# Kernel optimization log

Hardware: AMD Instinct MI355X
Metric: run time of the kernel (lower is better)

Reference implementation:

```python
import jax, jax.numpy as jnp
import numpy as np

NUM_GRAPHS = 256  # static batch size (= batch_indices.max()+1 by construction)
EMBED = 32
HIDDEN = 256
DEPTH = 10


def setup_inputs() -> dict:
    key = jax.random.key(0)
    ks = jax.random.split(key, 16)
    N, M = 8192, 16384
    atom_features = jax.random.randint(ks[0], (N,), 0, 200, dtype=jnp.int32)
    bond_features = jax.random.randint(ks[1], (M,), 0, 10, dtype=jnp.int32)
    adjacency_matrix = jax.random.randint(ks[2], (N, N), 0, 2, dtype=jnp.int32)
    batch_indices = jnp.sort(jax.random.randint(ks[3], (N,), 0, NUM_GRAPHS, dtype=jnp.int32))
    s = 0.05
    atom_emb_table = jax.random.normal(ks[4], (200, EMBED), jnp.float32) * s
    bond_emb_table = jax.random.normal(ks[5], (10, EMBED), jnp.float32) * s
    msg_W = jax.random.normal(ks[6], (DEPTH, HIDDEN, 2 * EMBED), jnp.float32) * s
    msg_b = jax.random.normal(ks[7], (DEPTH, HIDDEN), jnp.float32) * s
    gru_Wih = jax.random.normal(ks[8], (DEPTH, 3 * EMBED, HIDDEN), jnp.float32) * s
    gru_Whh = jax.random.normal(ks[9], (DEPTH, 3 * EMBED, EMBED), jnp.float32) * s
    gru_bih = jax.random.normal(ks[10], (DEPTH, 3 * EMBED), jnp.float32) * s
    gru_bhh = jax.random.normal(ks[11], (DEPTH, 3 * EMBED), jnp.float32) * s
    pool_W = jax.random.normal(ks[12], (HIDDEN, EMBED), jnp.float32) * s
    pool_b = jax.random.normal(ks[13], (HIDDEN,), jnp.float32) * s
    return dict(atom_features=atom_features, bond_features=bond_features,
                adjacency_matrix=adjacency_matrix, batch_indices=batch_indices,
                atom_emb_table=atom_emb_table, bond_emb_table=bond_emb_table,
                msg_W=msg_W, msg_b=msg_b, gru_Wih=gru_Wih, gru_Whh=gru_Whh,
                gru_bih=gru_bih, gru_bhh=gru_bhh, pool_W=pool_W, pool_b=pool_b)


def _gru_step(x, h, Wih, Whh, bih, bhh):
    # single-step torch-style GRU cell: x [N,HIDDEN], h [N,EMBED]
    gi = x @ Wih.T + bih                      # [N, 3E]
    gh = h @ Whh.T + bhh                      # [N, 3E]
    i_r, i_z, i_n = jnp.split(gi, 3, axis=-1)
    h_r, h_z, h_n = jnp.split(gh, 3, axis=-1)
    r = jax.nn.sigmoid(i_r + h_r)
    z = jax.nn.sigmoid(i_z + h_z)
    n = jnp.tanh(i_n + r * h_n)
    return (1.0 - z) * n + z * h


def reference(atom_features, bond_features, adjacency_matrix, batch_indices,
              atom_emb_table, bond_emb_table, msg_W, msg_b,
              gru_Wih, gru_Whh, gru_bih, gru_bhh, pool_W, pool_b):
    h = atom_emb_table[atom_features]                      # [N, E]
    A = (adjacency_matrix != 0).astype(h.dtype)            # [N, N]
    deg = A.sum(axis=-1, keepdims=True)                    # [N, 1]
    inv_deg = 1.0 / jnp.maximum(deg, 1.0)
    has_nei = deg > 0
    for d in range(DEPTH):
        # mean over neighbors of Linear(concat(self, nei)) == affine in (self, mean_nei)
        nei_mean = (A @ h) * inv_deg                       # [N, E]
        W_self = msg_W[d][:, :EMBED]                       # [H, E]
        W_nei = msg_W[d][:, EMBED:]                        # [H, E]
        msg = h @ W_self.T + nei_mean @ W_nei.T + msg_b[d]  # [N, H]
        msg = jnp.where(has_nei, msg, 0.0)                 # zero message if no neighbors
        h = _gru_step(msg, h, gru_Wih[d], gru_Whh[d], gru_bih[d], gru_bhh[d])
        # dropout is identity in eval mode
    # segment-mean pooling over graphs (zeros for empty graphs)
    sums = jax.ops.segment_sum(h, batch_indices, num_segments=NUM_GRAPHS)      # [B, E]
    counts = jax.ops.segment_sum(jnp.ones((h.shape[0],), h.dtype), batch_indices,
                                 num_segments=NUM_GRAPHS)[:, None]             # [B, 1]
    graph_mean = jnp.where(counts > 0, sums / jnp.maximum(counts, 1.0), 0.0)
    graph_embeddings = graph_mean @ pool_W.T + pool_b                          # [B, H]
    bond_embeddings = bond_emb_table[bond_features]                            # [M, E]
    return h, bond_embeddings, graph_embeddings
```

## Files before the change

kernel.cpp:

```cpp
#include <hip/hip_runtime.h>
#include <stdint.h>

#define N_ATOMS 8192
#define EMBED   32
#define DEPTHN  10

typedef short bf16x8 __attribute__((ext_vector_type(8)));
typedef float f32x4  __attribute__((ext_vector_type(4)));

__device__ __forceinline__ unsigned short f2bf(float f){
    unsigned u = __builtin_bit_cast(unsigned, f);
    u = u + 0x7FFFu + ((u >> 16) & 1u);
    return (unsigned short)(u >> 16);
}

__global__ __launch_bounds__(256) void k_preA(const int* __restrict__ A,
                                              unsigned long long* __restrict__ mask,
                                              int row0)
{
    const int i = row0 + blockIdx.x;
    const int t = threadIdx.x, w = t >> 6, l = t & 63;
    const int* row = A + (size_t)i * N_ATOMS;
    __shared__ unsigned long long lm[128];
    #pragma unroll
    for (int k = 0; k < 32; ++k){
        int j = k*256 + t;
        unsigned long long m = __ballot(row[j] != 0);
        if (l == 0) lm[k*4 + w] = m;
    }
    __syncthreads();
    if (t < 128) mask[(size_t)i*128 + t] = lm[t];
}

__global__ __launch_bounds__(256) void k_prep(
    const unsigned* __restrict__ maskRM, unsigned* __restrict__ mP,
    float* __restrict__ deg, float* __restrict__ invdeg,
    const int* __restrict__ af, const float* __restrict__ atom_emb,
    const float* __restrict__ msgW, const float* __restrict__ msgb,
    const float* __restrict__ Wih, const float* __restrict__ bih,
    float* __restrict__ hA, unsigned short* __restrict__ hP,
    float* __restrict__ Wc, float* __restrict__ bc,
    const int* __restrict__ bfeat, const float* __restrict__ bondf,
    float* __restrict__ out1)
{
    const int t = threadIdx.x;
    if (blockIdx.x < 512){
        const int grp = blockIdx.x;
        __shared__ unsigned lm[16*260];
        __shared__ int red[256];
        #pragma unroll
        for (int s = 0; s < 16; ++s)
            lm[s*260 + t] = maskRM[(size_t)grp*4096 + s*256 + t];
        __syncthreads();
        {
            int r = t >> 4, seg = t & 15, cnt = 0;
            #pragma unroll
            for (int k = 0; k < 16; ++k) cnt += __popc(lm[r*260 + seg*16 + k]);
            red[t] = cnt; __syncthreads();
            if (t < 16){
                int s = 0;
                #pragma unroll
                for (int k = 0; k < 16; ++k) s += red[t*16 + k];
                deg[grp*16 + t] = (float)s;
                invdeg[grp*16 + t] = 1.f / fmaxf((float)s, 1.f);
            }
        }
        unsigned* out = mP + (size_t)grp*4096;
        #pragma unroll
        for (int s = 0; s < 16; ++s){
            int W = s*256 + t;
            out[W] = lm[(W & 15)*260 + (W >> 4)];
        }
    } else {
        const int blk = blockIdx.x - 512;
        if (blk < 1024){
            int idx = blk*256 + t;
            int i = idx >> 5, e = idx & 31;
            float v = atom_emb[af[i]*EMBED + e];
            hA[idx] = v;
            int g = i >> 5, qd = (i >> 3) & 3, j8 = i & 7;
            hP[(size_t)((g*2 + (e>>4))*64 + qd*16 + (e&15))*8 + j8] = f2bf(v);
        } else if (blk < 1264){
            int o = (blk-1024)*256 + t;
            int d = o / 6144, r = o % 6144, g = r >> 6, e = r & 63;
            const float* wi = Wih  + (size_t)(d*96 + g)*256;
            const float* mw = msgW + (size_t)d*256*64 + e;
            float acc = 0.f;
            for (int hh = 0; hh < 256; ++hh) acc += wi[hh] * mw[hh*64];
            Wc[o] = acc;
        } else if (blk < 1268){
            int o = (blk-1264)*256 + t;
            if (o < 960){
                int d = o / 96;
                const float* wi = Wih + (size_t)o*256;
                const float* mb = msgb + d*256;
                float acc = 0.f;
                for (int hh = 0; hh < 256; ++hh) acc += wi[hh] * mb[hh];
                bc[o] = acc + bih[o];
            }
        } else {
            int idx = (blk-1268)*256 + t;
            out1[idx] = bondf[bfeat[idx >> 5]*EMBED + (idx & 31)];
        }
    }
}

__global__ __launch_bounds__(512) void k_depth(
    const unsigned short* __restrict__ hPin,
    const unsigned* __restrict__ mP,
    const float* __restrict__ hin, float* __restrict__ hout,
    const float* __restrict__ invdeg, const float* __restrict__ deg,
    const float* __restrict__ Wc, const float* __restrict__ bc,
    const float* __restrict__ bihf, const float* __restrict__ bhhf,
    const float* __restrict__ Whhf,
    unsigned short* __restrict__ hPout, float* __restrict__ out0, int last)
{
    __shared__ uint2 lut[16];
    __shared__ float part[8][32][33];
    __shared__ float xs[32][68];
    const int t = threadIdx.x, blk = blockIdx.x;
    if (t < 16){
        unsigned lo = ((t & 1) ? 0x3F80u : 0u) | ((t & 2) ? 0x3F800000u : 0u);
        unsigned hi = ((t & 4) ? 0x3F80u : 0u) | ((t & 8) ? 0x3F800000u : 0u);
        lut[t] = make_uint2(lo, hi);
    }
    __syncthreads();
    {
        const int q = t >> 6, lane = t & 63;
        const int n = lane & 15, quad = lane >> 4;
        const int rt0 = blk*2;
        f32x4 a00 = {0.f,0.f,0.f,0.f};
        f32x4 a01 = {0.f,0.f,0.f,0.f};
        f32x4 a10 = {0.f,0.f,0.f,0.f};
        f32x4 a11 = {0.f,0.f,0.f,0.f};
        const unsigned* m0 = mP + (size_t)rt0*4096 + n;
        const unsigned* m1 = m0 + 4096;
        #pragma unroll 4
        for (int kk = 0; kk < 32; ++kk){
            const int g = q*32 + kk;
            union { uint4 u; bf16x8 v; } b0, b1;
            b0.u = *(const uint4*)&hPin[(size_t)((g*2+0)*64 + lane)*8];
            b1.u = *(const uint4*)&hPin[(size_t)((g*2+1)*64 + lane)*8];
            unsigned by0 = (m0[g*16] >> (quad*8)) & 0xFFu;
            unsigned by1 = (m1[g*16] >> (quad*8)) & 0xFFu;
            union { uint2 d[2]; bf16x8 v; } af0, af1;
            af0.d[0] = lut[by0 & 15u];
            af0.d[1] = lut[by0 >> 4];
            af1.d[0] = lut[by1 & 15u];
            af1.d[1] = lut[by1 >> 4];
            a00 = __builtin_amdgcn_mfma_f32_16x16x32_bf16(af0.v, b0.v, a00, 0, 0, 0);
            a01 = __builtin_amdgcn_mfma_f32_16x16x32_bf16(af0.v, b1.v, a01, 0, 0, 0);
            a10 = __builtin_amdgcn_mfma_f32_16x16x32_bf16(af1.v, b0.v, a10, 0, 0, 0);
            a11 = __builtin_amdgcn_mfma_f32_16x16x32_bf16(af1.v, b1.v, a11, 0, 0, 0);
        }
        #pragma unroll
        for (int r = 0; r < 4; ++r){
            int rl = quad*4 + r;
            part[q][rl][n]       = a00[r];
            part[q][rl][16+n]    = a01[r];
            part[q][16+rl][n]    = a10[r];
            part[q][16+rl][16+n] = a11[r];
        }
    }
    __syncthreads();
    {
        #pragma unroll
        for (int ii = 0; ii < 2; ++ii){
            int i = ii*512 + t;
            int a = i >> 5, e = i & 31;
            float s = 0.f;
            #pragma unroll
            for (int q = 0; q < 8; ++q) s += part[q][a][e];
            xs[a][32+e] = s;
            xs[a][e] = hin[(size_t)blk*1024 + i];
        }
    }
    __syncthreads();
    {
        const int a = t & 15, pw = t >> 4;
        const int al = a + (pw & 16);
        const int p  = pw & 15;
        const int atom = blk*32 + al;
        const float idg = invdeg[atom];
        const bool nz = deg[atom] > 0.f;
        float x[64];
        #pragma unroll
        for (int r = 0; r < 16; ++r){
            float4 v = *(const float4*)&xs[al][r*4];
            x[r*4+0]=v.x; x[r*4+1]=v.y; x[r*4+2]=v.z; x[r*4+3]=v.w;
        }
        #pragma unroll
        for (int e = 32; e < 64; ++e) x[e] *= idg;
        const int gg = atom >> 5, qd = (atom >> 3) & 3, j8 = atom & 7;
        #pragma unroll
        for (int jj = 0; jj < 2; ++jj){
            const int j = p*2 + jj;
            const float* wr = Wc + j*64;
            const float* wz = Wc + (32+j)*64;
            const float* wn = Wc + (64+j)*64;
            float gr=0.f, gz=0.f, gn=0.f;
            #pragma unroll
            for (int e = 0; e < 64; ++e){ gr += wr[e]*x[e]; gz += wz[e]*x[e]; gn += wn[e]*x[e]; }
            if (nz){ gr += bc[j]; gz += bc[32+j]; gn += bc[64+j]; }
            else   { gr  = bihf[j]; gz = bihf[32+j]; gn = bihf[64+j]; }
            const float* vr = Whhf + j*32;
            const float* vz = Whhf + (32+j)*32;
            const float* vn = Whhf + (64+j)*32;
            float hr=bhhf[j], hz=bhhf[32+j], hn=bhhf[64+j];
            #pragma unroll
            for (int e = 0; e < 32; ++e){ hr += vr[e]*x[e]; hz += vz[e]*x[e]; hn += vn[e]*x[e]; }
            float rg = 1.f/(1.f + expf(-(gr+hr)));
            float zg = 1.f/(1.f + expf(-(gz+hz)));
            float ng = tanhf(gn + rg*hn);
            float hnew = (1.f - zg)*ng + zg*x[j];
            hout[(size_t)atom*EMBED + j] = hnew;
            hPout[(size_t)((gg*2 + (j>>4))*64 + qd*16 + (j&15))*8 + j8] = f2bf(hnew);
            if (last) out0[(size_t)atom*EMBED + j] = hnew;
        }
    }
}

__global__ __launch_bounds__(256) void k_pool(
    const float* __restrict__ h, const int* __restrict__ batch,
    const float* __restrict__ poolW, const float* __restrict__ poolb,
    float* __restrict__ out2)
{
    const int b = blockIdx.x, t = threadIdx.x;
    int lo, hi;
    { int l = 0, r = N_ATOMS; while (l < r){ int m = (l+r)>>1; if (batch[m] < b)   l = m+1; else r = m; } lo = l; }
    { int l = 0, r = N_ATOMS; while (l < r){ int m = (l+r)>>1; if (batch[m] < b+1) l = m+1; else r = m; } hi = l; }
    const int cnt = hi - lo;
    __shared__ float ps[8][32];
    __shared__ float mean[32];
    const int e = t & 31, g = t >> 5;
    float acc = 0.f;
    for (int a = lo + g; a < hi; a += 8) acc += h[(size_t)a*EMBED + e];
    ps[g][e] = acc; __syncthreads();
    if (t < 32){
        float s = 0.f;
        #pragma unroll
        for (int gg = 0; gg < 8; ++gg) s += ps[gg][t];
        mean[t] = (cnt > 0) ? s / (float)cnt : 0.f;
    }
    __syncthreads();
    float emb = poolb[t];
    #pragma unroll
    for (int ee = 0; ee < 32; ++ee) emb += mean[ee] * poolW[t*32 + ee];
    out2[b*256 + t] = emb;
}

extern "C" void kernel_launch(void* const* d_in, const int* in_sizes, int n_in,
                              void* d_out, int out_size, void* d_ws, size_t ws_size,
                              hipStream_t stream)
{
    (void)in_sizes; (void)n_in; (void)out_size;
    const int* af   = (const int*)d_in[0];
    const int* bfe  = (const int*)d_in[1];
    const int* A    = (const int*)d_in[2];
    const int* bidx = (const int*)d_in[3];
    const float* atom_emb = (const float*)d_in[4];
    const float* bond_emb = (const float*)d_in[5];
    const float* msgW  = (const float*)d_in[6];
    const float* msgb  = (const float*)d_in[7];
    const float* Wih   = (const float*)d_in[8];
    const float* Whh   = (const float*)d_in[9];
    const float* bih   = (const float*)d_in[10];
    const float* bhh   = (const float*)d_in[11];
    const float* poolW = (const float*)d_in[12];
    const float* poolb = (const float*)d_in[13];

    float* out0 = (float*)d_out;
    float* out1 = out0 + 262144;
    float* out2 = out1 + 524288;

    float* deg    = out2;
    float* invdeg = out2 + 8192;

    unsigned long long* maskRM;
    unsigned*       mP;
    float*          hA; float* hB; float* Wc; float* bc;
    unsigned short* hP0; unsigned short* hP1;
    const int wsok = (ws_size >= (size_t)33554432) ? 1 : 0;
    if (wsok){
        char* W = (char*)d_ws;
        maskRM  = (unsigned long long*)(W + 0);
        mP      = (unsigned*)(W + 8388608);
        hP0     = (unsigned short*)(W + 16777216);
        hA      = (float*)(W + 17825792);
        hB      = (float*)(W + 18874368);
        Wc      = (float*)(W + 19922944);
        bc      = (float*)(W + 20185088);
        hP1     = (unsigned short*)(W + 20971520);
        k_preA<<<dim3(8192), dim3(256), 0, stream>>>(A, maskRM, 0);
    } else {
        char* Ab = (char*)d_in[2];
        hA      = (float*)(Ab + 0);
        hB      = (float*)(Ab + 1048576);
        hP0     = (unsigned short*)(Ab + 2097152);
        Wc      = (float*)(Ab + 2621440);
        bc      = (float*)(Ab + 2867200);
        hP1     = (unsigned short*)(Ab + 4194304);
        mP      = (unsigned*)(Ab + 13631488);
        maskRM  = (unsigned long long*)(Ab + 260046848);
        k_preA<<<dim3(1),    dim3(256), 0, stream>>>(A, maskRM, 8191);
        k_preA<<<dim3(7),    dim3(256), 0, stream>>>(A, maskRM, 8184);
        k_preA<<<dim3(248),  dim3(256), 0, stream>>>(A, maskRM, 7936);
        k_preA<<<dim3(7936), dim3(256), 0, stream>>>(A, maskRM, 0);
    }
    k_prep<<<dim3(3828), dim3(256), 0, stream>>>((const unsigned*)maskRM, mP,
        deg, invdeg, af, atom_emb, msgW, msgb, Wih, bih, hA, hP0, Wc, bc,
        bfe, bond_emb, out1);

    float* hin = hA; float* hout = hB;
    unsigned short* hPi = hP0; unsigned short* hPo = hP1;
    for (int d = 0; d < DEPTHN; ++d){
        k_depth<<<dim3(256), dim3(512), 0, stream>>>(hPi, mP, hin, hout,
            invdeg, deg, Wc + d*6144, bc + d*96, bih + d*96, bhh + d*96,
            Whh + d*3072, hPo, out0, (d == DEPTHN-1) ? 1 : 0);
        float* tf = hin; hin = hout; hout = tf;
        unsigned short* tp = hPi; hPi = hPo; hPo = tp;
    }
    k_pool<<<dim3(256), dim3(256), 0, stream>>>(hin, bidx, poolW, poolb, out2);
}
```

Baseline: 669.0 us.

## Fuse prep, depth iterations and pooling into one cooperative persistent kernel

Replaces the prep kernel, ten per-depth kernels and the pooling kernel with a single cooperative kernel that uses grid-wide syncs between phases. Each block keeps its atoms' fp32 hidden state in shared memory across depths, so the fp32 h ping-pong buffers in global memory are no longer written and re-read. The aim is to remove launch gaps and per-depth global round-trips. In exchange, prep work (mask transpose, fused weights, bond lookup) now runs on only 256 blocks instead of thousands, and every phase boundary costs a grid barrier.

```diff
diff --git a/kernel.cpp b/kernel.cpp
--- a/kernel.cpp
+++ b/kernel.cpp
@@ -1,5 +1,8 @@
 #include <hip/hip_runtime.h>
+#include <hip/hip_cooperative_groups.h>
 #include <stdint.h>
+
+namespace cg = cooperative_groups;
 
 #define N_ATOMS 8192
 #define EMBED   32
@@ -32,31 +35,63 @@
     if (t < 128) mask[(size_t)i*128 + t] = lm[t];
 }
 
-__global__ __launch_bounds__(256) void k_prep(
+__global__ __launch_bounds__(512) void k_mega(
     const unsigned* __restrict__ maskRM, unsigned* __restrict__ mP,
     float* __restrict__ deg, float* __restrict__ invdeg,
     const int* __restrict__ af, const float* __restrict__ atom_emb,
     const float* __restrict__ msgW, const float* __restrict__ msgb,
     const float* __restrict__ Wih, const float* __restrict__ bih,
-    float* __restrict__ hA, unsigned short* __restrict__ hP,
+    unsigned short* __restrict__ hP0, unsigned short* __restrict__ hP1,
     float* __restrict__ Wc, float* __restrict__ bc,
     const int* __restrict__ bfeat, const float* __restrict__ bondf,
-    float* __restrict__ out1)
+    float* __restrict__ out1,
+    const float* __restrict__ Whh, const float* __restrict__ bhh,
+    const int* __restrict__ batch, const float* __restrict__ poolW,
+    const float* __restrict__ poolb,
+    float* __restrict__ out0, float* __restrict__ out2)
 {
-    const int t = threadIdx.x;
-    if (blockIdx.x < 512){
-        const int grp = blockIdx.x;
-        __shared__ unsigned lm[16*260];
-        __shared__ int red[256];
-        #pragma unroll
-        for (int s = 0; s < 16; ++s)
-            lm[s*260 + t] = maskRM[(size_t)grp*4096 + s*256 + t];
-        __syncthreads();
-        {
-            int r = t >> 4, seg = t & 15, cnt = 0;
-            #pragma unroll
-            for (int k = 0; k < 16; ++k) cnt += __popc(lm[r*260 + seg*16 + k]);
-            red[t] = cnt; __syncthreads();
+    cg::grid_group grid = cg::this_grid();
+    __shared__ float xs[32][68];
+    __shared__ __align__(16) char ovl[33920];
+    float (*part)[32][33] = (float (*)[32][33])ovl;
+    uint2* lutp = (uint2*)(ovl + 33792);
+    const int t = threadIdx.x, blk = blockIdx.x;
+
+    if (t < 16){
+        unsigned lo = ((t & 1) ? 0x3F80u : 0u) | ((t & 2) ? 0x3F800000u : 0u);
+        unsigned hi = ((t & 4) ? 0x3F80u : 0u) | ((t & 8) ? 0x3F800000u : 0u);
+        lutp[t] = make_uint2(lo, hi);
+    }
+
+    #pragma unroll
+    for (int k2 = 0; k2 < 2; ++k2){
+        int idx = k2*512 + t;
+        int il = idx >> 5, e = idx & 31;
+        int i = blk*32 + il;
+        float v = atom_emb[af[i]*EMBED + e];
+        xs[il][e] = v;
+        int g = i >> 5, qd = (i >> 3) & 3, j8 = i & 7;
+        hP0[(size_t)((g*2 + (e>>4))*64 + qd*16 + (e&15))*8 + j8] = f2bf(v);
+    }
+    {
+        unsigned* lm = (unsigned*)ovl;
+        int* red = (int*)(ovl + 16640);
+        for (int gi = 0; gi < 2; ++gi){
+            const int grp = blk*2 + gi;
+            __syncthreads();
+            #pragma unroll
+            for (int s8 = 0; s8 < 8; ++s8){
+                int idx = s8*512 + t;
+                lm[(idx >> 8)*260 + (idx & 255)] = maskRM[(size_t)grp*4096 + idx];
+            }
+            __syncthreads();
+            if (t < 256){
+                int r = t >> 4, seg = t & 15, cnt = 0;
+                #pragma unroll
+                for (int k = 0; k < 16; ++k) cnt += __popc(lm[r*260 + seg*16 + k]);
+                red[t] = cnt;
+            }
+            __syncthreads();
             if (t < 16){
                 int s = 0;
                 #pragma unroll
@@ -64,189 +99,176 @@
                 deg[grp*16 + t] = (float)s;
                 invdeg[grp*16 + t] = 1.f / fmaxf((float)s, 1.f);
             }
-        }
-        unsigned* out = mP + (size_t)grp*4096;
-        #pragma unroll
-        for (int s = 0; s < 16; ++s){
-            int W = s*256 + t;
-            out[W] = lm[(W & 15)*260 + (W >> 4)];
-        }
-    } else {
-        const int blk = blockIdx.x - 512;
-        if (blk < 1024){
-            int idx = blk*256 + t;
-            int i = idx >> 5, e = idx & 31;
-            float v = atom_emb[af[i]*EMBED + e];
-            hA[idx] = v;
-            int g = i >> 5, qd = (i >> 3) & 3, j8 = i & 7;
-            hP[(size_t)((g*2 + (e>>4))*64 + qd*16 + (e&15))*8 + j8] = f2bf(v);
-        } else if (blk < 1264){
-            int o = (blk-1024)*256 + t;
-            int d = o / 6144, r = o % 6144, g = r >> 6, e = r & 63;
-            const float* wi = Wih  + (size_t)(d*96 + g)*256;
-            const float* mw = msgW + (size_t)d*256*64 + e;
+            unsigned* outw = mP + (size_t)grp*4096;
+            #pragma unroll
+            for (int s8 = 0; s8 < 8; ++s8){
+                int W = s8*512 + t;
+                outw[W] = lm[(W & 15)*260 + (W >> 4)];
+            }
+        }
+    }
+    if (t < 240){
+        int o = blk*240 + t;
+        int d = o / 6144, r = o % 6144, g = r >> 6, e = r & 63;
+        const float* wi = Wih  + (size_t)(d*96 + g)*256;
+        const float* mw = msgW + (size_t)d*256*64 + e;
+        float acc = 0.f;
+        for (int hh = 0; hh < 256; ++hh) acc += wi[hh] * mw[hh*64];
+        Wc[o] = acc;
+    }
+    if (blk < 2 && t < 480){
+        int o = blk*480 + t;
+        if (o < 960){
+            int d = o / 96;
+            const float* wi = Wih + (size_t)o*256;
+            const float* mb = msgb + d*256;
             float acc = 0.f;
-            for (int hh = 0; hh < 256; ++hh) acc += wi[hh] * mw[hh*64];
-            Wc[o] = acc;
-        } else if (blk < 1268){
-            int o = (blk-1264)*256 + t;
-            if (o < 960){
-                int d = o / 96;
-                const float* wi = Wih + (size_t)o*256;
-                const float* mb = msgb + d*256;
-                float acc = 0.f;
-                for (int hh = 0; hh < 256; ++hh) acc += wi[hh] * mb[hh];
-                bc[o] = acc + bih[o];
-            }
-        } else {
-            int idx = (blk-1268)*256 + t;
-            out1[idx] = bondf[bfeat[idx >> 5]*EMBED + (idx & 31)];
-        }
-    }
-}
-
-__global__ __launch_bounds__(512) void k_depth(
-    const unsigned short* __restrict__ hPin,
-    const unsigned* __restrict__ mP,
-    const float* __restrict__ hin, float* __restrict__ hout,
-    const float* __restrict__ invdeg, const float* __restrict__ deg,
-    const float* __restrict__ Wc, const float* __restrict__ bc,
-    const float* __restrict__ bihf, const float* __restrict__ bhhf,
-    const float* __restrict__ Whhf,
-    unsigned short* __restrict__ hPout, float* __restrict__ out0, int last)
-{
-    __shared__ uint2 lut[16];
-    __shared__ float part[8][32][33];
-    __shared__ float xs[32][68];
-    const int t = threadIdx.x, blk = blockIdx.x;
-    if (t < 16){
-        unsigned lo = ((t & 1) ? 0x3F80u : 0u) | ((t & 2) ? 0x3F800000u : 0u);
-        unsigned hi = ((t & 4) ? 0x3F80u : 0u) | ((t & 8) ? 0x3F800000u : 0u);
-        lut[t] = make_uint2(lo, hi);
-    }
-    __syncthreads();
+            for (int hh = 0; hh < 256; ++hh) acc += wi[hh] * mb[hh];
+            bc[o] = acc + bih[o];
+        }
+    }
+    #pragma unroll
+    for (int k4 = 0; k4 < 4; ++k4){
+        int idx = blk*2048 + k4*512 + t;
+        out1[idx] = bondf[bfeat[idx >> 5]*EMBED + (idx & 31)];
+    }
+    grid.sync();
+
+    const int a_  = t & 15, pw = t >> 4;
+    const int al  = a_ + (pw & 16);
+    const int p   = pw & 15;
+    const int atom = blk*32 + al;
+    const float idg = invdeg[atom];
+    const bool nz = deg[atom] > 0.f;
+    const int ggp = atom >> 5, qdp = (atom >> 3) & 3, j8p = atom & 7;
+
+    unsigned short* hPi = hP0;
+    unsigned short* hPo = hP1;
+    for (int d = 0; d < DEPTHN; ++d){
+        const float* Wcd  = Wc  + d*6144;
+        const float* bcd  = bc  + d*96;
+        const float* bihf = bih + d*96;
+        const float* bhhf = bhh + d*96;
+        const float* Whhf = Whh + d*3072;
+        {
+            const int q = t >> 6, lane = t & 63;
+            const int n = lane & 15, quad = lane >> 4;
+            const int rt0 = blk*2;
+            f32x4 a00 = {0.f,0.f,0.f,0.f};
+            f32x4 a01 = {0.f,0.f,0.f,0.f};
+            f32x4 a10 = {0.f,0.f,0.f,0.f};
+            f32x4 a11 = {0.f,0.f,0.f,0.f};
+            const unsigned* m0 = mP + (size_t)rt0*4096 + n;
+            const unsigned* m1 = m0 + 4096;
+            #pragma unroll 4
+            for (int kk = 0; kk < 32; ++kk){
+                const int g = q*32 + kk;
+                union { uint4 u; bf16x8 v; } b0, b1;
+                b0.u = *(const uint4*)&hPi[(size_t)((g*2+0)*64 + lane)*8];
+                b1.u = *(const uint4*)&hPi[(size_t)((g*2+1)*64 + lane)*8];
+                unsigned by0 = (m0[g*16] >> (quad*8)) & 0xFFu;
+                unsigned by1 = (m1[g*16] >> (quad*8)) & 0xFFu;
+                union { uint2 dd[2]; bf16x8 v; } af0, af1;
+                af0.dd[0] = lutp[by0 & 15u];
+                af0.dd[1] = lutp[by0 >> 4];
+                af1.dd[0] = lutp[by1 & 15u];
+                af1.dd[1] = lutp[by1 >> 4];
+                a00 = __builtin_amdgcn_mfma_f32_16x16x32_bf16(af0.v, b0.v, a00, 0, 0, 0);
+                a01 = __builtin_amdgcn_mfma_f32_16x16x32_bf16(af0.v, b1.v, a01, 0, 0, 0);
+                a10 = __builtin_amdgcn_mfma_f32_16x16x32_bf16(af1.v, b0.v, a10, 0, 0, 0);
+                a11 = __builtin_amdgcn_mfma_f32_16x16x32_bf16(af1.v, b1.v, a11, 0, 0, 0);
+            }
+            #pragma unroll
+            for (int r = 0; r < 4; ++r){
+                int rl = quad*4 + r;
+                part[q][rl][n]       = a00[r];
+                part[q][rl][16+n]    = a01[r];
+                part[q][16+rl][n]    = a10[r];
+                part[q][16+rl][16+n] = a11[r];
+            }
+        }
+        __syncthreads();
+        {
+            #pragma unroll
+            for (int ii = 0; ii < 2; ++ii){
+                int i = ii*512 + t;
+                int a2 = i >> 5, e = i & 31;
+                float s = 0.f;
+                #pragma unroll
+                for (int q2 = 0; q2 < 8; ++q2) s += part[q2][a2][e];
+                xs[a2][32+e] = s;
+            }
+        }
+        __syncthreads();
+        {
+            float x[64];
+            #pragma unroll
+            for (int r = 0; r < 16; ++r){
+                float4 v = *(const float4*)&xs[al][r*4];
+                x[r*4+0]=v.x; x[r*4+1]=v.y; x[r*4+2]=v.z; x[r*4+3]=v.w;
+            }
+            #pragma unroll
+            for (int e = 32; e < 64; ++e) x[e] *= idg;
+            __syncthreads();
+            #pragma unroll
+            for (int jj = 0; jj < 2; ++jj){
+                const int j = p*2 + jj;
+                const float* wr = Wcd + j*64;
+                const float* wz = Wcd + (32+j)*64;
+                const float* wn = Wcd + (64+j)*64;
+                float gr=0.f, gz=0.f, gn=0.f;
+                #pragma unroll
+                for (int e = 0; e < 64; ++e){ gr += wr[e]*x[e]; gz += wz[e]*x[e]; gn += wn[e]*x[e]; }
+                if (nz){ gr += bcd[j]; gz += bcd[32+j]; gn += bcd[64+j]; }
+                else   { gr  = bihf[j]; gz = bihf[32+j]; gn = bihf[64+j]; }
+                const float* vr = Whhf + j*32;
+                const float* vz = Whhf + (32+j)*32;
+                const float* vn = Whhf + (64+j)*32;
+                float hr=bhhf[j], hz=bhhf[32+j], hn=bhhf[64+j];
+                #pragma unroll
+                for (int e = 0; e < 32; ++e){ hr += vr[e]*x[e]; hz += vz[e]*x[e]; hn += vn[e]*x[e]; }
+                float rg = 1.f/(1.f + expf(-(gr+hr)));
+                float zg = 1.f/(1.f + expf(-(gz+hz)));
+                float ng = tanhf(gn + rg*hn);
+                float hnew = (1.f - zg)*ng + zg*x[j];
+                xs[al][j] = hnew;
+                hPo[(size_t)((ggp*2 + (j>>4))*64 + qdp*16 + (j&15))*8 + j8p] = f2bf(hnew);
+                if (d == DEPTHN-1) out0[(size_t)atom*EMBED + j] = hnew;
+            }
+        }
+        grid.sync();
+        unsigned short* tp = hPi; hPi = hPo; hPo = tp;
+    }
+
     {
-        const int q = t >> 6, lane = t & 63;
-        const int n = lane & 15, quad = lane >> 4;
-        const int rt0 = blk*2;
-        f32x4 a00 = {0.f,0.f,0.f,0.f};
-        f32x4 a01 = {0.f,0.f,0.f,0.f};
-        f32x4 a10 = {0.f,0.f,0.f,0.f};
-        f32x4 a11 = {0.f,0.f,0.f,0.f};
-        const unsigned* m0 = mP + (size_t)rt0*4096 + n;
-        const unsigned* m1 = m0 + 4096;
-        #pragma unroll 4
-        for (int kk = 0; kk < 32; ++kk){
-            const int g = q*32 + kk;
-            union { uint4 u; bf16x8 v; } b0, b1;
-            b0.u = *(const uint4*)&hPin[(size_t)((g*2+0)*64 + lane)*8];
-            b1.u = *(const uint4*)&hPin[(size_t)((g*2+1)*64 + lane)*8];
-            unsigned by0 = (m0[g*16] >> (quad*8)) & 0xFFu;
-            unsigned by1 = (m1[g*16] >> (quad*8)) & 0xFFu;
-            union { uint2 d[2]; bf16x8 v; } af0, af1;
-            af0.d[0] = lut[by0 & 15u];
-            af0.d[1] = lut[by0 >> 4];
-            af1.d[0] = lut[by1 & 15u];
-            af1.d[1] = lut[by1 >> 4];
-            a00 = __builtin_amdgcn_mfma_f32_16x16x32_bf16(af0.v, b0.v, a00, 0, 0, 0);
-            a01 = __builtin_amdgcn_mfma_f32_16x16x32_bf16(af0.v, b1.v, a01, 0, 0, 0);
-            a10 = __builtin_amdgcn_mfma_f32_16x16x32_bf16(af1.v, b0.v, a10, 0, 0, 0);
-            a11 = __builtin_amdgcn_mfma_f32_16x16x32_bf16(af1.v, b1.v, a11, 0, 0, 0);
-        }
-        #pragma unroll
-        for (int r = 0; r < 4; ++r){
-            int rl = quad*4 + r;
-            part[q][rl][n]       = a00[r];
-            part[q][rl][16+n]    = a01[r];
-            part[q][16+rl][n]    = a10[r];
-            part[q][16+rl][16+n] = a11[r];
-        }
-    }
-    __syncthreads();
-    {
-        #pragma unroll
-        for (int ii = 0; ii < 2; ++ii){
-            int i = ii*512 + t;
-            int a = i >> 5, e = i & 31;
+        const int b = blk;
+        int lo, hi;
+        { int l = 0, r = N_ATOMS; while (l < r){ int m = (l+r)>>1; if (batch[m] < b)   l = m+1; else r = m; } lo = l; }
+        { int l = 0, r = N_ATOMS; while (l < r){ int m = (l+r)>>1; if (batch[m] < b+1) l = m+1; else r = m; } hi = l; }
+        const int cnt = hi - lo;
+        float* ps   = (float*)ovl;
+        float* mean = (float*)(ovl + 1024);
+        const int e = t & 31, g = (t >> 5) & 7;
+        if (t < 256){
+            float acc = 0.f;
+            for (int a2 = lo + g; a2 < hi; a2 += 8) acc += out0[(size_t)a2*EMBED + e];
+            ps[g*32 + e] = acc;
+        }
+        __syncthreads();
+        if (t < 32){
             float s = 0.f;
             #pragma unroll
-            for (int q = 0; q < 8; ++q) s += part[q][a][e];
-            xs[a][32+e] = s;
-            xs[a][e] = hin[(size_t)blk*1024 + i];
-        }
-    }
-    __syncthreads();
-    {
-        const int a = t & 15, pw = t >> 4;
-        const int al = a + (pw & 16);
-        const int p  = pw & 15;
-        const int atom = blk*32 + al;
-        const float idg = invdeg[atom];
-        const bool nz = deg[atom] > 0.f;
-        float x[64];
-        #pragma unroll
-        for (int r = 0; r < 16; ++r){
-            float4 v = *(const float4*)&xs[al][r*4];
-            x[r*4+0]=v.x; x[r*4+1]=v.y; x[r*4+2]=v.z; x[r*4+3]=v.w;
-        }
-        #pragma unroll
-        for (int e = 32; e < 64; ++e) x[e] *= idg;
-        const int gg = atom >> 5, qd = (atom >> 3) & 3, j8 = atom & 7;
-        #pragma unroll
-        for (int jj = 0; jj < 2; ++jj){
-            const int j = p*2 + jj;
-            const float* wr = Wc + j*64;
-            const float* wz = Wc + (32+j)*64;
-            const float* wn = Wc + (64+j)*64;
-            float gr=0.f, gz=0.f, gn=0.f;
-            #pragma unroll
-            for (int e = 0; e < 64; ++e){ gr += wr[e]*x[e]; gz += wz[e]*x[e]; gn += wn[e]*x[e]; }
-            if (nz){ gr += bc[j]; gz += bc[32+j]; gn += bc[64+j]; }
-            else   { gr  = bihf[j]; gz = bihf[32+j]; gn = bihf[64+j]; }
-            const float* vr = Whhf + j*32;
-            const float* vz = Whhf + (32+j)*32;
-            const float* vn = Whhf + (64+j)*32;
-            float hr=bhhf[j], hz=bhhf[32+j], hn=bhhf[64+j];
-            #pragma unroll
-            for (int e = 0; e < 32; ++e){ hr += vr[e]*x[e]; hz += vz[e]*x[e]; hn += vn[e]*x[e]; }
-            float rg = 1.f/(1.f + expf(-(gr+hr)));
-            float zg = 1.f/(1.f + expf(-(gz+hz)));
-            float ng = tanhf(gn + rg*hn);
-            float hnew = (1.f - zg)*ng + zg*x[j];
-            hout[(size_t)atom*EMBED + j] = hnew;
-            hPout[(size_t)((gg*2 + (j>>4))*64 + qd*16 + (j&15))*8 + j8] = f2bf(hnew);
-            if (last) out0[(size_t)atom*EMBED + j] = hnew;
-        }
-    }
-}
-
-__global__ __launch_bounds__(256) void k_pool(
-    const float* __restrict__ h, const int* __restrict__ batch,
-    const float* __restrict__ poolW, const float* __restrict__ poolb,
-    float* __restrict__ out2)
-{
-    const int b = blockIdx.x, t = threadIdx.x;
-    int lo, hi;
-    { int l = 0, r = N_ATOMS; while (l < r){ int m = (l+r)>>1; if (batch[m] < b)   l = m+1; else r = m; } lo = l; }
-    { int l = 0, r = N_ATOMS; while (l < r){ int m = (l+r)>>1; if (batch[m] < b+1) l = m+1; else r = m; } hi = l; }
-    const int cnt = hi - lo;
-    __shared__ float ps[8][32];
-    __shared__ float mean[32];
-    const int e = t & 31, g = t >> 5;
-    float acc = 0.f;
-    for (int a = lo + g; a < hi; a += 8) acc += h[(size_t)a*EMBED + e];
-    ps[g][e] = acc; __syncthreads();
-    if (t < 32){
-        float s = 0.f;
-        #pragma unroll
-        for (int gg = 0; gg < 8; ++gg) s += ps[gg][t];
-        mean[t] = (cnt > 0) ? s / (float)cnt : 0.f;
-    }
-    __syncthreads();
-    float emb = poolb[t];
-    #pragma unroll
-    for (int ee = 0; ee < 32; ++ee) emb += mean[ee] * poolW[t*32 + ee];
-    out2[b*256 + t] = emb;
+            for (int gg2 = 0; gg2 < 8; ++gg2) s += ps[gg2*32 + t];
+            mean[t] = (cnt > 0) ? s / (float)cnt : 0.f;
+        }
+        __syncthreads();
+        if (t < 256){
+            float emb = poolb[t];
+            #pragma unroll
+            for (int ee = 0; ee < 32; ++ee) emb += mean[ee] * poolW[t*32 + ee];
+            out2[b*256 + t] = emb;
+        }
+    }
 }
 
 extern "C" void kernel_launch(void* const* d_in, const int* in_sizes, int n_in,
@@ -278,7 +300,7 @@
 
     unsigned long long* maskRM;
     unsigned*       mP;
-    float*          hA; float* hB; float* Wc; float* bc;
+    float*          Wc; float* bc;
     unsigned short* hP0; unsigned short* hP1;
     const int wsok = (ws_size >= (size_t)33554432) ? 1 : 0;
     if (wsok){
@@ -286,16 +308,12 @@
         maskRM  = (unsigned long long*)(W + 0);
         mP      = (unsigned*)(W + 8388608);
         hP0     = (unsigned short*)(W + 16777216);
-        hA      = (float*)(W + 17825792);
-        hB      = (float*)(W + 18874368);
         Wc      = (float*)(W + 19922944);
         bc      = (float*)(W + 20185088);
         hP1     = (unsigned short*)(W + 20971520);
         k_preA<<<dim3(8192), dim3(256), 0, stream>>>(A, maskRM, 0);
     } else {
         char* Ab = (char*)d_in[2];
-        hA      = (float*)(Ab + 0);
-        hB      = (float*)(Ab + 1048576);
         hP0     = (unsigned short*)(Ab + 2097152);
         Wc      = (float*)(Ab + 2621440);
         bc      = (float*)(Ab + 2867200);
@@ -307,18 +325,16 @@
         k_preA<<<dim3(248),  dim3(256), 0, stream>>>(A, maskRM, 7936);
         k_preA<<<dim3(7936), dim3(256), 0, stream>>>(A, maskRM, 0);
     }
-    k_prep<<<dim3(3828), dim3(256), 0, stream>>>((const unsigned*)maskRM, mP,
-        deg, invdeg, af, atom_emb, msgW, msgb, Wih, bih, hA, hP0, Wc, bc,
-        bfe, bond_emb, out1);
-
-    float* hin = hA; float* hout = hB;
-    unsigned short* hPi = hP0; unsigned short* hPo = hP1;
-    for (int d = 0; d < DEPTHN; ++d){
-        k_depth<<<dim3(256), dim3(512), 0, stream>>>(hPi, mP, hin, hout,
-            invdeg, deg, Wc + d*6144, bc + d*96, bih + d*96, bhh + d*96,
-            Whh + d*3072, hPo, out0, (d == DEPTHN-1) ? 1 : 0);
-        float* tf = hin; hin = hout; hout = tf;
-        unsigned short* tp = hPi; hPi = hPo; hPo = tp;
-    }
-    k_pool<<<dim3(256), dim3(256), 0, stream>>>(hin, bidx, poolW, poolb, out2);
+
+    const unsigned* maskRMu = (const unsigned*)maskRM;
+    void* kargs[] = {
+        (void*)&maskRMu, (void*)&mP, (void*)&deg, (void*)&invdeg,
+        (void*)&af, (void*)&atom_emb, (void*)&msgW, (void*)&msgb,
+        (void*)&Wih, (void*)&bih, (void*)&hP0, (void*)&hP1,
+        (void*)&Wc, (void*)&bc, (void*)&bfe, (void*)&bond_emb,
+        (void*)&out1, (void*)&Whh, (void*)&bhh, (void*)&bidx,
+        (void*)&poolW, (void*)&poolb, (void*)&out0, (void*)&out2
+    };
+    hipLaunchCooperativeKernel((void*)k_mega, dim3(256), dim3(512),
+                               kargs, 0, stream);
 }
```

New measurement: 992.3 us. 1.48x slower.

## Fuse adjacency bitmask extraction with mask packing and preprocessing into one kernel

Applied to the files above, without the earlier changes.

Adds a k_pre2 kernel that reads each adjacency row, builds the ballot bitmask, computes the degree and inverse degree, and writes the bits directly into the packed MFMA mask layout. The same launch also does the embedding, folded-weight and bond preprocessing. This removes the intermediate row-major mask buffer round-trip and one kernel launch on the workspace path. In exchange, per-row degree reduction adds syncs, and the packed-layout stores are scattered (stride 16 words).

```diff
diff --git a/kernel.cpp b/kernel.cpp
--- a/kernel.cpp
+++ b/kernel.cpp
@@ -30,6 +30,82 @@
     }
     __syncthreads();
     if (t < 128) mask[(size_t)i*128 + t] = lm[t];
+}
+
+__global__ __launch_bounds__(256) void k_pre2(
+    const int* __restrict__ A, unsigned* __restrict__ mP,
+    float* __restrict__ deg, float* __restrict__ invdeg,
+    const int* __restrict__ af, const float* __restrict__ atom_emb,
+    const float* __restrict__ msgW, const float* __restrict__ msgb,
+    const float* __restrict__ Wih, const float* __restrict__ bih,
+    float* __restrict__ hA, unsigned short* __restrict__ hP,
+    float* __restrict__ Wc, float* __restrict__ bc,
+    const int* __restrict__ bfeat, const float* __restrict__ bondf,
+    float* __restrict__ out1)
+{
+    const int t = threadIdx.x;
+    __shared__ unsigned lm[256];
+    __shared__ int red[4];
+    if (blockIdx.x < 8192){
+        const int blk = blockIdx.x;
+        const int grp = (blk >> 7)*8 + (blk & 7);
+        const int n   = (blk >> 3) & 15;
+        const int i   = grp*16 + n;
+        const int w = t >> 6, l = t & 63;
+        const int* row = A + (size_t)i * N_ATOMS;
+        #pragma unroll
+        for (int k = 0; k < 32; ++k){
+            int j = k*256 + t;
+            unsigned long long m = __ballot(row[j] != 0);
+            if (l == 0){
+                lm[(k*4 + w)*2]     = (unsigned)m;
+                lm[(k*4 + w)*2 + 1] = (unsigned)(m >> 32);
+            }
+        }
+        __syncthreads();
+        int cnt = __popc(lm[t]);
+        #pragma unroll
+        for (int off = 32; off >= 1; off >>= 1) cnt += __shfl_down(cnt, off, 64);
+        if (l == 0) red[w] = cnt;
+        __syncthreads();
+        if (t == 0){
+            int s = red[0] + red[1] + red[2] + red[3];
+            deg[i] = (float)s;
+            invdeg[i] = 1.f / fmaxf((float)s, 1.f);
+        }
+        mP[(size_t)grp*4096 + t*16 + n] = lm[t];
+    } else {
+        const int blk = blockIdx.x - 8192;
+        if (blk < 1024){
+            int idx = blk*256 + t;
+            int i = idx >> 5, e = idx & 31;
+            float v = atom_emb[af[i]*EMBED + e];
+            hA[idx] = v;
+            int g = i >> 5, qd = (i >> 3) & 3, j8 = i & 7;
+            hP[(size_t)((g*2 + (e>>4))*64 + qd*16 + (e&15))*8 + j8] = f2bf(v);
+        } else if (blk < 1264){
+            int o = (blk-1024)*256 + t;
+            int d = o / 6144, r = o % 6144, g = r >> 6, e = r & 63;
+            const float* wi = Wih  + (size_t)(d*96 + g)*256;
+            const float* mw = msgW + (size_t)d*256*64 + e;
+            float acc = 0.f;
+            for (int hh = 0; hh < 256; ++hh) acc += wi[hh] * mw[hh*64];
+            Wc[o] = acc;
+        } else if (blk < 1268){
+            int o = (blk-1264)*256 + t;
+            if (o < 960){
+                int d = o / 96;
+                const float* wi = Wih + (size_t)o*256;
+                const float* mb = msgb + d*256;
+                float acc = 0.f;
+                for (int hh = 0; hh < 256; ++hh) acc += wi[hh] * mb[hh];
+                bc[o] = acc + bih[o];
+            }
+        } else {
+            int idx = (blk-1268)*256 + t;
+            out1[idx] = bondf[bfeat[idx >> 5]*EMBED + (idx & 31)];
+        }
+    }
 }
 
 __global__ __launch_bounds__(256) void k_prep(
@@ -143,11 +219,11 @@
             b1.u = *(const uint4*)&hPin[(size_t)((g*2+1)*64 + lane)*8];
             unsigned by0 = (m0[g*16] >> (quad*8)) & 0xFFu;
             unsigned by1 = (m1[g*16] >> (quad*8)) & 0xFFu;
-            union { uint2 d[2]; bf16x8 v; } af0, af1;
-            af0.d[0] = lut[by0 & 15u];
-            af0.d[1] = lut[by0 >> 4];
-            af1.d[0] = lut[by1 & 15u];
-            af1.d[1] = lut[by1 >> 4];
+            union { uint2 dd[2]; bf16x8 v; } af0, af1;
+            af0.dd[0] = lut[by0 & 15u];
+            af0.dd[1] = lut[by0 >> 4];
+            af1.dd[0] = lut[by1 & 15u];
+            af1.dd[1] = lut[by1 >> 4];
             a00 = __builtin_amdgcn_mfma_f32_16x16x32_bf16(af0.v, b0.v, a00, 0, 0, 0);
             a01 = __builtin_amdgcn_mfma_f32_16x16x32_bf16(af0.v, b1.v, a01, 0, 0, 0);
             a10 = __builtin_amdgcn_mfma_f32_16x16x32_bf16(af1.v, b0.v, a10, 0, 0, 0);
@@ -276,14 +352,12 @@
     float* deg    = out2;
     float* invdeg = out2 + 8192;
 
-    unsigned long long* maskRM;
     unsigned*       mP;
     float*          hA; float* hB; float* Wc; float* bc;
     unsigned short* hP0; unsigned short* hP1;
     const int wsok = (ws_size >= (size_t)33554432) ? 1 : 0;
     if (wsok){
         char* W = (char*)d_ws;
-        maskRM  = (unsigned long long*)(W + 0);
         mP      = (unsigned*)(W + 8388608);
         hP0     = (unsigned short*)(W + 16777216);
         hA      = (float*)(W + 17825792);
@@ -291,8 +365,11 @@
         Wc      = (float*)(W + 19922944);
         bc      = (float*)(W + 20185088);
         hP1     = (unsigned short*)(W + 20971520);
-        k_preA<<<dim3(8192), dim3(256), 0, stream>>>(A, maskRM, 0);
+        k_pre2<<<dim3(11508), dim3(256), 0, stream>>>(A, mP, deg, invdeg,
+            af, atom_emb, msgW, msgb, Wih, bih, hA, hP0, Wc, bc,
+            bfe, bond_emb, out1);
     } else {
+        unsigned long long* maskRM;
         char* Ab = (char*)d_in[2];
         hA      = (float*)(Ab + 0);
         hB      = (float*)(Ab + 1048576);
@@ -306,10 +383,10 @@
         k_preA<<<dim3(7),    dim3(256), 0, stream>>>(A, maskRM, 8184);
         k_preA<<<dim3(248),  dim3(256), 0, stream>>>(A, maskRM, 7936);
         k_preA<<<dim3(7936), dim3(256), 0, stream>>>(A, maskRM, 0);
-    }
-    k_prep<<<dim3(3828), dim3(256), 0, stream>>>((const unsigned*)maskRM, mP,
-        deg, invdeg, af, atom_emb, msgW, msgb, Wih, bih, hA, hP0, Wc, bc,
-        bfe, bond_emb, out1);
+        k_prep<<<dim3(3828), dim3(256), 0, stream>>>((const unsigned*)maskRM, mP,
+            deg, invdeg, af, atom_emb, msgW, msgb, Wih, bih, hA, hP0, Wc, bc,
+            bfe, bond_emb, out1);
+    }
 
     float* hin = hA; float* hout = hB;
     unsigned short* hPi = hP0; unsigned short* hPo = hP1;
```

Result: no change. 666.5 us, median of 2 (-0.4%).
